# Kernel optimization log

Measured on AMD Instinct MI355X. Metric: run time of the kernel, lower is better.

The kernel has to match this reference:

```python
import jax, jax.numpy as jnp
import numpy as np

B, S, D, H = 2, 2048, 1024, 16
HEAD_DIM = D // H
SCALE = HEAD_DIM ** -0.5


def setup_inputs() -> dict:
    key = jax.random.key(0)
    k1, k2, k3 = jax.random.split(key, 3)
    x = jax.random.normal(k1, (B, S, D), dtype=jnp.float32)
    # torch nn.Linear convention: weight is [out_features, in_features], y = x @ W.T + b
    W_qkv = jax.random.normal(k2, (3 * D, D), dtype=jnp.float32) * 0.02  # qkv Linear, bias=False
    W_out = jax.random.normal(k3, (D, D), dtype=jnp.float32) * 0.02
    b_out = jnp.zeros((D,), dtype=jnp.float32)
    return {"x": x, "W_qkv": W_qkv, "W_out": W_out, "b_out": b_out}


def reference(x, W_qkv, W_out, b_out):
    b, s, d_model = x.shape
    # qkv projection (no bias), then split 'b c (qkv h d) -> qkv b h c d'
    qkv = (x @ W_qkv.T).reshape(b, s, 3, H, HEAD_DIM).transpose(2, 0, 3, 1, 4)
    q, k, v = qkv[0], qkv[1], qkv[2]  # each [b, h, s, hd]
    # naive full attention: scores materialized as [b, h, s, s]
    attn = jax.nn.softmax(jnp.einsum('bhxd,bhyd->bhxy', q, k) * SCALE, axis=-1)
    # dropout is identity (rate 0 / eval mode)
    o = jnp.einsum('bhxy,bhyd->bhxd', attn, v)
    o = o.transpose(0, 2, 1, 3).reshape(b, s, d_model)  # 'b h c d -> b c (h d)'
    return o @ W_out.T + b_out
```

## Files before the change

kernel.cpp:

```cpp
#include <hip/hip_runtime.h>


typedef __attribute__((ext_vector_type(8))) short short8;
typedef __attribute__((ext_vector_type(4))) float f32x4;
typedef unsigned short ushort_t;
typedef unsigned int uint32;

#define AS1 __attribute__((address_space(1)))
#define AS3 __attribute__((address_space(3)))

__device__ __forceinline__ void gload_lds16(const void* gp, void* lp) {
    __builtin_amdgcn_global_load_lds((const AS1 void*)gp, (AS3 void*)lp, 16, 0, 0);
}

#if __has_builtin(__builtin_amdgcn_exp2f)
#define EXP2F(x) __builtin_amdgcn_exp2f(x)
#else
#define EXP2F(x) exp2f(x)
#endif

__device__ __forceinline__ uint32 rhu(float f) { return __float_as_uint(f) + 0x8000u; }
#if __has_builtin(__builtin_amdgcn_perm)
__device__ __forceinline__ uint32 pk2bf(float a, float b) {
    return __builtin_amdgcn_perm(rhu(b), rhu(a), 0x07060302u);
}
#else
__device__ __forceinline__ uint32 pk2bf(float a, float b) {
    return (rhu(a) >> 16) | (rhu(b) & 0xffff0000u);
}
#endif
__device__ __forceinline__ ushort_t f2bf(float f) { return (ushort_t)(rhu(f) >> 16); }

__global__ void cvt_all(const float* __restrict__ x, ushort_t* __restrict__ xb,
                        const float* __restrict__ wq, ushort_t* __restrict__ wqb,
                        const float* __restrict__ wo, ushort_t* __restrict__ wob) {
    int blk = blockIdx.x;
    const float* in; ushort_t* out;
    if (blk < 4096)      { in = x;  out = xb;  }
    else if (blk < 7168) { in = wq; out = wqb; blk -= 4096; }
    else                 { in = wo; out = wob; blk -= 7168; }
    const int i = (blk * 256 + threadIdx.x) * 4;
    const float4 v = *(const float4*)(in + i);
    uint2 pk;
    pk.x = pk2bf(v.x, v.y);
    pk.y = pk2bf(v.z, v.w);
    *(uint2*)(out + i) = pk;
}

__global__ __launch_bounds__(256, 2)
void gemm_qkv(const ushort_t* __restrict__ A, const ushort_t* __restrict__ B,
              ushort_t* __restrict__ Cb, ushort_t* __restrict__ vT,
              int M, int N, int K, int ldc, float qScale) {
    __shared__ ushort_t lA[2][128 * 32];
    __shared__ ushort_t lB[2][128 * 32];
    const int tid = threadIdx.x;
    const int wave = tid >> 6, lane = tid & 63;
    const int quad = lane >> 4, l16 = lane & 15;
    const int wr = wave >> 1, wc = wave & 1;
    const int mBase = blockIdx.y * 128, nBase = blockIdx.x * 128;

    f32x4 acc[4][4];
#pragma unroll
    for (int i = 0; i < 4; i++)
#pragma unroll
        for (int j = 0; j < 4; j++) acc[i][j] = (f32x4){0.f, 0.f, 0.f, 0.f};

    const int ar = tid >> 2;
    const int ac = (((tid & 3) ^ ((ar >> 1) & 3)) * 8);
    const int rsw = ((l16 >> 1) & 3);

    const ushort_t* aptr = A + (size_t)(mBase + ar) * K + ac;
    const ushort_t* bptr = B + (size_t)(nBase + ar) * K + ac;

#define G1_STAGE(buf, k0)                                                            \
    {                                                                                \
        _Pragma("unroll") for (int c = 0; c < 2; c++) {                              \
            gload_lds16(aptr + (size_t)(c * 64) * K + (k0), lA[buf] + c * 2048 + wave * 512); \
            gload_lds16(bptr + (size_t)(c * 64) * K + (k0), lB[buf] + c * 2048 + wave * 512); \
        }                                                                            \
    }

    G1_STAGE(0, 0);
    for (int k0 = 0; k0 < K; k0 += 32) {
        const int cur = (k0 >> 5) & 1;
        __syncthreads();
        if (k0 + 32 < K) G1_STAGE(cur ^ 1, k0 + 32);

        short8 af[4], bf[4];
#pragma unroll
        for (int i = 0; i < 4; i++)
            af[i] = *(const short8*)(lA[cur] + (wr * 64 + i * 16 + l16) * 32 + ((quad ^ rsw) * 8));
#pragma unroll
        for (int j = 0; j < 4; j++)
            bf[j] = *(const short8*)(lB[cur] + (wc * 64 + j * 16 + l16) * 32 + ((quad ^ rsw) * 8));
#pragma unroll
        for (int i = 0; i < 4; i++)
#pragma unroll
            for (int j = 0; j < 4; j++)
                acc[i][j] = __builtin_amdgcn_mfma_f32_16x16x32_bf16(af[i], bf[j], acc[i][j], 0, 0, 0);
    }

    if (nBase >= 2048) {
#pragma unroll
        for (int i = 0; i < 4; i++)
#pragma unroll
            for (int j = 0; j < 4; j++) {
                const int row0 = mBase + wr * 64 + i * 16 + quad * 4;
                const int col = nBase + wc * 64 + j * 16 + l16 - 2048;
                const int b = row0 >> 11, s0 = row0 & 2047;
                uint2 pk;
                pk.x = pk2bf(acc[i][j][0], acc[i][j][1]);
                pk.y = pk2bf(acc[i][j][2], acc[i][j][3]);
                *(uint2*)(vT + ((size_t)(b * 16) * 64 + col) * 2048 + s0) = pk;
            }
        return;
    }
    const float cs = (nBase < 1024) ? qScale : 1.0f;
#pragma unroll
    for (int i = 0; i < 4; i++)
#pragma unroll
        for (int j = 0; j < 4; j++)
#pragma unroll
            for (int r = 0; r < 4; r++) {
                const int row = mBase + wr * 64 + i * 16 + quad * 4 + r;
                const int col = nBase + wc * 64 + j * 16 + l16;
                Cb[(size_t)row * ldc + col] = f2bf(acc[i][j][r] * cs);
            }
}

__global__ __launch_bounds__(256, 2)
void gemm_out(const ushort_t* __restrict__ A, const ushort_t* __restrict__ B,
              float* __restrict__ Cf, const float* __restrict__ bias,
              int M, int N, int K) {
    __shared__ ushort_t lA[2][64 * 64];
    __shared__ ushort_t lB[2][128 * 64];
    const int tid = threadIdx.x;
    const int wave = tid >> 6, lane = tid & 63;
    const int quad = lane >> 4, l16 = lane & 15;
    const int mBase = blockIdx.y * 64, nBase = blockIdx.x * 128;

    f32x4 acc[4][2];
#pragma unroll
    for (int i = 0; i < 4; i++)
#pragma unroll
        for (int j = 0; j < 2; j++) acc[i][j] = (f32x4){0.f, 0.f, 0.f, 0.f};

    const int sr = tid >> 3;
    const int sc = ((tid & 7) ^ (sr & 7)) * 8;
    const int swz = l16 & 7;

    const ushort_t* aptr = A + (size_t)(mBase + sr) * K + sc;
    const ushort_t* bptr = B + (size_t)(nBase + sr) * K + sc;

#define G2_STAGE(buf, k0)                                                              \
    {                                                                                  \
        _Pragma("unroll") for (int c = 0; c < 2; c++)                                  \
            gload_lds16(aptr + (size_t)(c * 32) * K + (k0), lA[buf] + c * 2048 + wave * 512); \
        _Pragma("unroll") for (int c = 0; c < 4; c++)                                  \
            gload_lds16(bptr + (size_t)(c * 32) * K + (k0), lB[buf] + c * 2048 + wave * 512); \
    }

    G2_STAGE(0, 0);
    for (int k0 = 0; k0 < K; k0 += 64) {
        const int cur = (k0 >> 6) & 1;
        __syncthreads();
        if (k0 + 64 < K) G2_STAGE(cur ^ 1, k0 + 64);

#pragma unroll
        for (int ks = 0; ks < 2; ks++) {
            short8 af[4], bf[2];
#pragma unroll
            for (int i = 0; i < 4; i++)
                af[i] = *(const short8*)(lA[cur] + (i * 16 + l16) * 64 + (((ks * 4 + quad) ^ swz) * 8));
#pragma unroll
            for (int j = 0; j < 2; j++)
                bf[j] = *(const short8*)(lB[cur] + (wave * 32 + j * 16 + l16) * 64 + (((ks * 4 + quad) ^ swz) * 8));
#pragma unroll
            for (int i = 0; i < 4; i++)
#pragma unroll
                for (int j = 0; j < 2; j++)
                    acc[i][j] = __builtin_amdgcn_mfma_f32_16x16x32_bf16(af[i], bf[j], acc[i][j], 0, 0, 0);
        }
    }

#pragma unroll
    for (int i = 0; i < 4; i++)
#pragma unroll
        for (int j = 0; j < 2; j++)
#pragma unroll
            for (int r = 0; r < 4; r++) {
                const int row = mBase + i * 16 + quad * 4 + r;
                const int col = nBase + wave * 32 + j * 16 + l16;
                Cf[(size_t)row * N + col] = acc[i][j][r] + bias[col];
            }
}

__global__ __launch_bounds__(512, 4)
void attn_flash(const ushort_t* __restrict__ qk, const ushort_t* __restrict__ vT,
                ushort_t* __restrict__ o) {
    __shared__ ushort_t smem[26624];

    const int tid = threadIdx.x;
    const int wave = tid >> 6, lane = tid & 63;
    const int quad = lane >> 4, l16 = lane & 15;
    const int qg = wave & 3, kg = wave >> 2;
    const int bh = blockIdx.y, b = bh >> 4, h = bh & 15;
    const size_t rowBase = (size_t)b * 2048;
    const int qCol = h * 64, kCol = 1024 + h * 64;
    const int qRow0 = blockIdx.x * 128;
    const int swz = l16 & 7;

    ushort_t* lP = smem + 16384 + wave * 1280;

    const int sr = tid >> 3;
    const int sc = ((tid & 7) ^ (sr & 7)) * 8;

#pragma unroll
    for (int cc = 0; cc < 2; cc++)
        gload_lds16(qk + (rowBase + qRow0 + cc * 64 + sr) * 2048 + qCol + sc,
                    smem + 16384 + cc * 4096 + wave * 512);
    __syncthreads();
    short8 qf[2][2];
#pragma unroll
    for (int qt = 0; qt < 2; qt++)
#pragma unroll
        for (int ks = 0; ks < 2; ks++)
            qf[qt][ks] = *(const short8*)(smem + 16384 + (qg * 32 + qt * 16 + l16) * 64 +
                                          (((ks * 4 + quad) ^ swz) * 8));

    short8 onesA;
#pragma unroll
    for (int i = 0; i < 8; i++) onesA[i] = (short)0x3F80;

    f32x4 oacc[4][2];
    f32x4 lacc[2];
#pragma unroll
    for (int qt = 0; qt < 2; qt++) {
        lacc[qt] = (f32x4){0.f, 0.f, 0.f, 0.f};
#pragma unroll
        for (int dt = 0; dt < 4; dt++) oacc[dt][qt] = (f32x4){0.f, 0.f, 0.f, 0.f};
    }

    const ushort_t* kptr = qk + (rowBase + sr) * 2048 + kCol + sc;
    const ushort_t* vptr = vT + ((size_t)bh * 64 + sr) * 2048 + sc;

#define AT_STAGE(buf, kt)                                                              \
    {                                                                                  \
        gload_lds16(kptr + (size_t)((kt) * 64) * 2048,                                 \
                    smem + (buf) * 4096 + wave * 512);                                 \
        gload_lds16(vptr + (kt) * 64,                                                  \
                    smem + 8192 + (buf) * 4096 + wave * 512);                          \
    }

    AT_STAGE(0, 0);
    for (int kt = 0; kt < 32; kt++) {
        const int cur = kt & 1;
        __syncthreads();
        if (kt < 31) AT_STAGE(cur ^ 1, kt + 1);
        const ushort_t* lK = smem + cur * 4096;
        const ushort_t* lV = smem + 8192 + cur * 4096;

        f32x4 sacc[2][2];
#pragma unroll
        for (int mh = 0; mh < 2; mh++) {
            const int krow = kg * 32 + mh * 16 + l16;
            const short8 k0 = *(const short8*)(lK + krow * 64 + ((quad ^ swz) * 8));
            const short8 k1 = *(const short8*)(lK + krow * 64 + (((4 + quad) ^ swz) * 8));
            __builtin_amdgcn_s_setprio(1);
#pragma unroll
            for (int qt = 0; qt < 2; qt++) {
                f32x4 t = (f32x4){0.f, 0.f, 0.f, 0.f};
                t = __builtin_amdgcn_mfma_f32_16x16x32_bf16(k0, qf[qt][0], t, 0, 0, 0);
                t = __builtin_amdgcn_mfma_f32_16x16x32_bf16(k1, qf[qt][1], t, 0, 0, 0);
                sacc[mh][qt] = t;
            }
            __builtin_amdgcn_s_setprio(0);
        }

#pragma unroll
        for (int qt = 0; qt < 2; qt++)
#pragma unroll
            for (int mh = 0; mh < 2; mh++) {
                const f32x4 s = sacc[mh][qt];
                uint2 pk;
                pk.x = pk2bf(EXP2F(s[0]), EXP2F(s[1]));
                pk.y = pk2bf(EXP2F(s[2]), EXP2F(s[3]));
                *(uint2*)(&lP[(qt * 16 + l16) * 40 + mh * 16 + quad * 4]) = pk;
            }

        short8 pf[2];
#pragma unroll
        for (int qt = 0; qt < 2; qt++) {
            pf[qt] = *(const short8*)(&lP[(qt * 16 + l16) * 40 + quad * 8]);
            lacc[qt] = __builtin_amdgcn_mfma_f32_16x16x32_bf16(onesA, pf[qt], lacc[qt], 0, 0, 0);
        }
        __builtin_amdgcn_s_setprio(1);
#pragma unroll
        for (int dt = 0; dt < 4; dt++) {
            const short8 vf = *(const short8*)(lV + (dt * 16 + l16) * 64 +
                                               (((kg * 4 + quad) ^ swz) * 8));
#pragma unroll
            for (int qt = 0; qt < 2; qt++)
                oacc[dt][qt] = __builtin_amdgcn_mfma_f32_16x16x32_bf16(vf, pf[qt], oacc[dt][qt], 0, 0, 0);
        }
        __builtin_amdgcn_s_setprio(0);
    }

    __syncthreads();
    float* red = (float*)smem;
    if (kg == 1) {
#pragma unroll
        for (int qt = 0; qt < 2; qt++) {
            if (quad == 0) red[8192 + qg * 32 + qt * 16 + l16] = lacc[qt][0];
#pragma unroll
            for (int dt = 0; dt < 4; dt++)
                *(f32x4*)(red + (((qg * 4 + dt) * 2 + qt) * 64 + lane) * 4) = oacc[dt][qt];
        }
    }
    __syncthreads();
    if (kg == 0) {
        float linv[2];
#pragma unroll
        for (int qt = 0; qt < 2; qt++)
            linv[qt] = 1.0f / (lacc[qt][0] + red[8192 + qg * 32 + qt * 16 + l16]);
#pragma unroll
        for (int qt = 0; qt < 2; qt++) {
            const size_t row = rowBase + qRow0 + qg * 32 + qt * 16 + l16;
#pragma unroll
            for (int dt = 0; dt < 4; dt++) {
                const f32x4 r = *(const f32x4*)(red + (((qg * 4 + dt) * 2 + qt) * 64 + lane) * 4);
                uint2 pk;
                pk.x = pk2bf((oacc[dt][qt][0] + r[0]) * linv[qt],
                             (oacc[dt][qt][1] + r[1]) * linv[qt]);
                pk.y = pk2bf((oacc[dt][qt][2] + r[2]) * linv[qt],
                             (oacc[dt][qt][3] + r[3]) * linv[qt]);
                *(uint2*)(o + row * 1024 + h * 64 + dt * 16 + quad * 4) = pk;
            }
        }
    }
}

extern "C" void kernel_launch(void* const* d_in, const int* in_sizes, int n_in,
                              void* d_out, int out_size, void* d_ws, size_t ws_size,
                              hipStream_t stream) {
    const float* x    = (const float*)d_in[0];
    const float* Wqkv = (const float*)d_in[1];
    const float* Wout = (const float*)d_in[2];
    const float* bout = (const float*)d_in[3];
    float* out = (float*)d_out;

    ushort_t* xb    = (ushort_t*)d_ws;
    ushort_t* wqkvb = xb + (size_t)4096 * 1024;
    ushort_t* woutb = wqkvb + (size_t)3072 * 1024;
    ushort_t* qkb   = woutb + (size_t)1024 * 1024;
    ushort_t* vTb   = qkb + (size_t)4096 * 2048;
    ushort_t* ob    = xb;

    const float SC = 0.125f * 1.44269504089f;

    cvt_all<<<8192, 256, 0, stream>>>(x, xb, Wqkv, wqkvb, Wout, woutb);
    gemm_qkv<<<dim3(24, 32), 256, 0, stream>>>(xb, wqkvb, qkb, vTb, 4096, 3072, 1024, 2048, SC);
    attn_flash<<<dim3(16, 32), 512, 0, stream>>>(qkb, vTb, ob);
    gemm_out<<<dim3(8, 64), 256, 0, stream>>>(ob, woutb, out, bout, 4096, 1024, 1024);
}
```

Baseline: 175.4 us.

## Software-pipeline attention loop by overlapping QK^T of next tile with PV of previous

```diff
diff --git a/kernel.cpp b/kernel.cpp
--- a/kernel.cpp
+++ b/kernel.cpp
@@ -198,7 +198,7 @@
 __global__ __launch_bounds__(512, 4)
 void attn_flash(const ushort_t* __restrict__ qk, const ushort_t* __restrict__ vT,
                 ushort_t* __restrict__ o) {
-    __shared__ ushort_t smem[26624];
+    __shared__ ushort_t smem[30720];
 
     const int tid = threadIdx.x;
     const int wave = tid >> 6, lane = tid & 63;
@@ -210,7 +210,7 @@
     const int qRow0 = blockIdx.x * 128;
     const int swz = l16 & 7;
 
-    ushort_t* lP = smem + 16384 + wave * 1280;
+    ushort_t* lP = smem + 20480 + wave * 1280;
 
     const int sr = tid >> 3;
     const int sc = ((tid & 7) ^ (sr & 7)) * 8;
@@ -218,14 +218,14 @@
 #pragma unroll
     for (int cc = 0; cc < 2; cc++)
         gload_lds16(qk + (rowBase + qRow0 + cc * 64 + sr) * 2048 + qCol + sc,
-                    smem + 16384 + cc * 4096 + wave * 512);
+                    smem + 20480 + cc * 4096 + wave * 512);
     __syncthreads();
     short8 qf[2][2];
 #pragma unroll
     for (int qt = 0; qt < 2; qt++)
 #pragma unroll
         for (int ks = 0; ks < 2; ks++)
-            qf[qt][ks] = *(const short8*)(smem + 16384 + (qg * 32 + qt * 16 + l16) * 64 +
+            qf[qt][ks] = *(const short8*)(smem + 20480 + (qg * 32 + qt * 16 + l16) * 64 +
                                           (((ks * 4 + quad) ^ swz) * 8));
 
     short8 onesA;
@@ -244,67 +244,84 @@
     const ushort_t* kptr = qk + (rowBase + sr) * 2048 + kCol + sc;
     const ushort_t* vptr = vT + ((size_t)bh * 64 + sr) * 2048 + sc;
 
-#define AT_STAGE(buf, kt)                                                              \
+    f32x4 sacc[2][2];
+
+#define AT_STAGE(kbi, vbi, kt)                                                         \
     {                                                                                  \
-        gload_lds16(kptr + (size_t)((kt) * 64) * 2048,                                 \
-                    smem + (buf) * 4096 + wave * 512);                                 \
-        gload_lds16(vptr + (kt) * 64,                                                  \
-                    smem + 8192 + (buf) * 4096 + wave * 512);                          \
-    }
-
-    AT_STAGE(0, 0);
-    for (int kt = 0; kt < 32; kt++) {
-        const int cur = kt & 1;
+        gload_lds16(kptr + (size_t)((kt) * 64) * 2048, smem + (kbi) * 4096 + wave * 512); \
+        gload_lds16(vptr + (kt) * 64, smem + 8192 + (vbi) * 4096 + wave * 512);        \
+    }
+
+#define S_BLOCK(cur)                                                                   \
+    {                                                                                  \
+        const ushort_t* lK = smem + (cur) * 4096;                                      \
+        _Pragma("unroll") for (int mh = 0; mh < 2; mh++) {                             \
+            const int krow = kg * 32 + mh * 16 + l16;                                  \
+            const short8 k0 = *(const short8*)(lK + krow * 64 + ((quad ^ swz) * 8));   \
+            const short8 k1 = *(const short8*)(lK + krow * 64 + (((4 + quad) ^ swz) * 8)); \
+            __builtin_amdgcn_s_setprio(1);                                             \
+            _Pragma("unroll") for (int qt = 0; qt < 2; qt++) {                         \
+                f32x4 t = (f32x4){0.f, 0.f, 0.f, 0.f};                                 \
+                t = __builtin_amdgcn_mfma_f32_16x16x32_bf16(k0, qf[qt][0], t, 0, 0, 0); \
+                t = __builtin_amdgcn_mfma_f32_16x16x32_bf16(k1, qf[qt][1], t, 0, 0, 0); \
+                sacc[mh][qt] = t;                                                      \
+            }                                                                          \
+            __builtin_amdgcn_s_setprio(0);                                             \
+        }                                                                              \
+    }
+
+#define EXP_BLOCK()                                                                    \
+    _Pragma("unroll") for (int qt = 0; qt < 2; qt++)                                   \
+        _Pragma("unroll") for (int mh = 0; mh < 2; mh++) {                             \
+            const f32x4 s = sacc[mh][qt];                                              \
+            uint2 pk;                                                                  \
+            pk.x = pk2bf(EXP2F(s[0]), EXP2F(s[1]));                                    \
+            pk.y = pk2bf(EXP2F(s[2]), EXP2F(s[3]));                                    \
+            *(uint2*)(&lP[(qt * 16 + l16) * 40 + mh * 16 + quad * 4]) = pk;            \
+        }
+
+#define PV_BLOCK(vbi)                                                                  \
+    {                                                                                  \
+        const ushort_t* lV = smem + 8192 + (vbi) * 4096;                               \
+        short8 pf[2];                                                                  \
+        _Pragma("unroll") for (int qt = 0; qt < 2; qt++) {                             \
+            pf[qt] = *(const short8*)(&lP[(qt * 16 + l16) * 40 + quad * 8]);           \
+            lacc[qt] = __builtin_amdgcn_mfma_f32_16x16x32_bf16(onesA, pf[qt], lacc[qt], 0, 0, 0); \
+        }                                                                              \
+        __builtin_amdgcn_s_setprio(1);                                                 \
+        _Pragma("unroll") for (int dt = 0; dt < 4; dt++) {                             \
+            const short8 vf = *(const short8*)(lV + (dt * 16 + l16) * 64 +             \
+                                               (((kg * 4 + quad) ^ swz) * 8));         \
+            _Pragma("unroll") for (int qt = 0; qt < 2; qt++)                           \
+                oacc[dt][qt] = __builtin_amdgcn_mfma_f32_16x16x32_bf16(vf, pf[qt], oacc[dt][qt], 0, 0, 0); \
+        }                                                                              \
+        __builtin_amdgcn_s_setprio(0);                                                 \
+    }
+
+    AT_STAGE(0, 0, 0);
+
+    __syncthreads();
+    AT_STAGE(1, 1, 1);
+    S_BLOCK(0);
+    EXP_BLOCK();
+
+    int vs = 2;
+    int vp = 0;
+    for (int kt = 1; kt <= 30; ++kt) {
         __syncthreads();
-        if (kt < 31) AT_STAGE(cur ^ 1, kt + 1);
-        const ushort_t* lK = smem + cur * 4096;
-        const ushort_t* lV = smem + 8192 + cur * 4096;
-
-        f32x4 sacc[2][2];
-#pragma unroll
-        for (int mh = 0; mh < 2; mh++) {
-            const int krow = kg * 32 + mh * 16 + l16;
-            const short8 k0 = *(const short8*)(lK + krow * 64 + ((quad ^ swz) * 8));
-            const short8 k1 = *(const short8*)(lK + krow * 64 + (((4 + quad) ^ swz) * 8));
-            __builtin_amdgcn_s_setprio(1);
-#pragma unroll
-            for (int qt = 0; qt < 2; qt++) {
-                f32x4 t = (f32x4){0.f, 0.f, 0.f, 0.f};
-                t = __builtin_amdgcn_mfma_f32_16x16x32_bf16(k0, qf[qt][0], t, 0, 0, 0);
-                t = __builtin_amdgcn_mfma_f32_16x16x32_bf16(k1, qf[qt][1], t, 0, 0, 0);
-                sacc[mh][qt] = t;
-            }
-            __builtin_amdgcn_s_setprio(0);
-        }
-
-#pragma unroll
-        for (int qt = 0; qt < 2; qt++)
-#pragma unroll
-            for (int mh = 0; mh < 2; mh++) {
-                const f32x4 s = sacc[mh][qt];
-                uint2 pk;
-                pk.x = pk2bf(EXP2F(s[0]), EXP2F(s[1]));
-                pk.y = pk2bf(EXP2F(s[2]), EXP2F(s[3]));
-                *(uint2*)(&lP[(qt * 16 + l16) * 40 + mh * 16 + quad * 4]) = pk;
-            }
-
-        short8 pf[2];
-#pragma unroll
-        for (int qt = 0; qt < 2; qt++) {
-            pf[qt] = *(const short8*)(&lP[(qt * 16 + l16) * 40 + quad * 8]);
-            lacc[qt] = __builtin_amdgcn_mfma_f32_16x16x32_bf16(onesA, pf[qt], lacc[qt], 0, 0, 0);
-        }
-        __builtin_amdgcn_s_setprio(1);
-#pragma unroll
-        for (int dt = 0; dt < 4; dt++) {
-            const short8 vf = *(const short8*)(lV + (dt * 16 + l16) * 64 +
-                                               (((kg * 4 + quad) ^ swz) * 8));
-#pragma unroll
-            for (int qt = 0; qt < 2; qt++)
-                oacc[dt][qt] = __builtin_amdgcn_mfma_f32_16x16x32_bf16(vf, pf[qt], oacc[dt][qt], 0, 0, 0);
-        }
-        __builtin_amdgcn_s_setprio(0);
-    }
+        AT_STAGE((kt + 1) & 1, vs, kt + 1);
+        S_BLOCK(kt & 1);
+        PV_BLOCK(vp);
+        EXP_BLOCK();
+        vs = (vs == 2) ? 0 : vs + 1;
+        vp = (vp == 2) ? 0 : vp + 1;
+    }
+
+    __syncthreads();
+    S_BLOCK(1);
+    PV_BLOCK(0);
+    EXP_BLOCK();
+    PV_BLOCK(1);
 
     __syncthreads();
     float* red = (float*)smem;
```

Result: no change. 175.5 us (+0.0%).
